# Kernel tuning notes

Hardware: AMD Instinct MI355X
Metric: run time of the kernel (lower is better)

The kernel has to match this reference:

```python
import jax, jax.numpy as jnp
import numpy as np

H = 12  # num_heads

def _alibi_bias(num_heads, n, dtype):
    # slopes: ratio**i for i in 1..H, ratio = 2**(-8/H)
    ratio = 2.0 ** (-8.0 / num_heads)
    slopes = ratio ** jnp.arange(1, num_heads + 1, dtype=jnp.float32)  # [H]
    pos = jnp.arange(n)
    rel = jnp.abs(pos[None, :] - pos[:, None]).astype(jnp.float32)  # [N,N]
    return (-slopes[:, None, None] * rel[None]).astype(dtype)  # [H,N,N]

def setup_inputs() -> dict:
    key = jax.random.key(0)
    ks = jax.random.split(key, 5)
    B, N, C = 16, 1024, 768
    s = 0.02
    return {
        "x": jax.random.normal(ks[0], (B, N, C), jnp.float32),
        "w_qkv": jax.random.normal(ks[1], (3 * C, C), jnp.float32) * s,
        "b_qkv": jax.random.normal(ks[2], (3 * C,), jnp.float32) * s,
        "w_proj": jax.random.normal(ks[3], (C, C), jnp.float32) * s,
        "b_proj": jax.random.normal(ks[4], (C,), jnp.float32) * s,
    }

def reference(x, w_qkv, b_qkv, w_proj, b_proj):
    B, N, C = x.shape
    D = C // H
    scale = D ** -0.5
    qkv = x @ w_qkv.T + b_qkv                       # [B,N,3C]
    qkv = qkv.reshape(B, N, 3, H, D)
    q = qkv[:, :, 0].transpose(0, 2, 1, 3)          # [B,H,N,D]
    k = qkv[:, :, 1].transpose(0, 2, 1, 3)
    v = qkv[:, :, 2].transpose(0, 2, 1, 3)
    bias = _alibi_bias(H, N, x.dtype)               # [H,N,N]
    scores = jnp.einsum('bhnd,bhmd->bhnm', q, k) * scale + bias[None]
    attn = jax.nn.softmax(scores, axis=-1)
    out = jnp.einsum('bhnm,bhmd->bhnd', attn, v)    # [B,H,N,D]
    out = out.transpose(0, 2, 1, 3).reshape(B, N, C)
    return out @ w_proj.T + b_proj
```

## Files before the change

### kernel.cpp

```cpp
#include <hip/hip_runtime.h>


typedef unsigned short u16;
typedef unsigned int u32;
typedef __attribute__((ext_vector_type(8))) short short8;
typedef __attribute__((ext_vector_type(4))) float f32x4;

__device__ __forceinline__ u16 f2bf(float f) {
    u32 u = __float_as_uint(f);
    u32 r = u + 0x7FFFu + ((u >> 16) & 1u);
    return (u16)(r >> 16);
}

__device__ __forceinline__ f32x4 mfma16(short8 a, short8 b, f32x4 c) {
    return __builtin_amdgcn_mfma_f32_16x16x32_bf16(a, b, c, 0, 0, 0);
}
__device__ __forceinline__ u32 cvtpk_bf16(float lo, float hi) {
    u32 r;
    asm("v_cvt_pk_bf16_f32 %0, %1, %2" : "=v"(r) : "v"(lo), "v"(hi));
    return r;
}

typedef __attribute__((address_space(1))) const unsigned int gu32_t;
typedef __attribute__((address_space(3))) unsigned int su32_t;
__device__ __forceinline__ void gl16(const u16* g, u16* s) {
    __builtin_amdgcn_global_load_lds((gu32_t*)g, (su32_t*)s, 16, 0, 0);
}

__global__ void cvt_all(const float* __restrict__ x, const float* __restrict__ wq,
                        const float* __restrict__ wp, u16* __restrict__ Xb,
                        u16* __restrict__ Wqkvb, u16* __restrict__ Wprojb) {
    int i = blockIdx.x * blockDim.x + threadIdx.x;
    int stride = gridDim.x * blockDim.x;
    for (int idx = i; idx < 3735552; idx += stride) {
        const float* src;
        u16* dst;
        int k;
        if (idx < 3145728) { src = x; dst = Xb; k = idx; }
        else if (idx < 3588096) { src = wq; dst = Wqkvb; k = idx - 3145728; }
        else { src = wp; dst = Wprojb; k = idx - 3588096; }
        float4 v = *(const float4*)(src + (size_t)k * 4);
        ushort4 o;
        o.x = f2bf(v.x); o.y = f2bf(v.y); o.z = f2bf(v.z); o.w = f2bf(v.w);
        *(ushort4*)(dst + (size_t)k * 4) = o;
    }
}

template <int EPI>
__global__ __launch_bounds__(512) void gemm_nt(
    const u16* __restrict__ A, const u16* __restrict__ Bw,
    const float* __restrict__ bias, u16* __restrict__ outb, float* __restrict__ outf,
    int nTilesN)
{
    constexpr int K = 768;
    constexpr int nkt = K / 32;
    __shared__ __align__(16) u16 lA[3][128 * 32];
    __shared__ __align__(16) u16 lB[3][128 * 32];

    int tid = threadIdx.x;
    int bid = blockIdx.x;
    int nwg = gridDim.x;
    int cpx = nwg >> 3;
    int swz = (bid & 7) * cpx + (bid >> 3);
    int bm = swz / nTilesN;
    int bn = swz - bm * nTilesN;
    int m0 = bm * 128, n0 = bn * 128;

    int sr = tid >> 2;
    int sc = (((tid & 3) ^ ((sr >> 1) & 3)) << 3);
    const u16* pA = A + (size_t)(m0 + sr) * K + sc;
    const u16* pB = Bw + (size_t)(n0 + sr) * K + sc;
    int lo = tid * 8;

    gl16(pA,      &lA[0][lo]);
    gl16(pB,      &lB[0][lo]);
    gl16(pA + 32, &lA[1][lo]);
    gl16(pB + 32, &lB[1][lo]);

    int w = tid >> 6, lane = tid & 63;
    int wm = w >> 2, wn = w & 3;
    int fq = lane >> 4, fr = lane & 15;
    int fsw = (fr >> 1) & 3;
    int colA = (fq ^ fsw) << 3;
    f32x4 acc[4][2] = {};

    for (int kt = 0; kt < nkt; ++kt) {
        int cur = kt % 3;
        if (kt < nkt - 1) { asm volatile("s_waitcnt vmcnt(2)" ::: "memory"); }
        else              { asm volatile("s_waitcnt vmcnt(0)" ::: "memory"); }
        __builtin_amdgcn_sched_barrier(0);
        __builtin_amdgcn_s_barrier();
        __builtin_amdgcn_sched_barrier(0);
        if (kt + 2 < nkt) {
            int nx = (kt + 2) % 3;
            gl16(pA + (kt + 2) * 32, &lA[nx][lo]);
            gl16(pB + (kt + 2) * 32, &lB[nx][lo]);
        }
        short8 af[4], bfr[2];
#pragma unroll
        for (int i = 0; i < 4; ++i)
            af[i] = *(const short8*)&lA[cur][(wm * 64 + i * 16 + fr) * 32 + colA];
#pragma unroll
        for (int j = 0; j < 2; ++j)
            bfr[j] = *(const short8*)&lB[cur][(wn * 32 + j * 16 + fr) * 32 + colA];
        __builtin_amdgcn_s_setprio(1);
#pragma unroll
        for (int i = 0; i < 4; ++i)
#pragma unroll
            for (int j = 0; j < 2; ++j)
                acc[i][j] = mfma16(af[i], bfr[j], acc[i][j]);
        __builtin_amdgcn_s_setprio(0);
    }

    if (EPI == 0) {
        int b = m0 >> 10;
        int i0 = (m0 & 1023) + wm * 64;
#pragma unroll
        for (int j = 0; j < 2; ++j) {
            int colb = n0 + wn * 32 + j * 16;
            int s = colb / 768;
            int rem = colb % 768;
            int hh = rem >> 6;
            int d0 = rem & 63;
            float bval = bias[colb + fr];
            u16* obase = outb + (((size_t)s * 16 + b) * 12 + hh) * 65536;
#pragma unroll
            for (int i = 0; i < 4; ++i) {
                int r0 = i0 + i * 16 + fq * 4;
#pragma unroll
                for (int r = 0; r < 4; ++r)
                    obase[(size_t)(r0 + r) * 64 + d0 + fr] = f2bf(acc[i][j][r] + bval);
            }
        }
    } else {
#pragma unroll
        for (int j = 0; j < 2; ++j) {
            int col = n0 + wn * 32 + j * 16 + fr;
            float bval = bias[col];
#pragma unroll
            for (int i = 0; i < 4; ++i) {
                int row0 = m0 + wm * 64 + i * 16 + fq * 4;
#pragma unroll
                for (int r = 0; r < 4; ++r)
                    outf[(size_t)(row0 + r) * 768 + col] = acc[i][j][r] + bval;
            }
        }
    }
}

__global__ __launch_bounds__(512) void attn_alibi(
    const u16* __restrict__ QKV, u16* __restrict__ att)
{
    int g = blockIdx.x;
    int xcd = g & 7;
    int idx = g >> 3;
    int qt = idx & 7;
    int bh = xcd * 24 + (idx >> 3);
    int h = bh % 12;
    int b = bh / 12;
    int q0 = qt * 128;
    const u16* Qg = QKV + (size_t)bh * 65536;
    const u16* Kg = QKV + (size_t)(192 + bh) * 65536;
    const u16* Vg = QKV + (size_t)(384 + bh) * 65536;

    __shared__ __align__(16) u16 Ks[64][72];
    __shared__ __align__(16) u16 Vt[64][72];
    __shared__ __align__(16) u16 Ps[128][72];

    int tid = threadIdx.x, w = tid >> 6, lane = tid & 63;
    int fq = lane >> 4, fr = lane & 15;

    short8 aq0 = *(const short8*)(Qg + (size_t)(q0 + w * 16 + fr) * 64 + fq * 8);
    short8 aq1 = *(const short8*)(Qg + (size_t)(q0 + w * 16 + fr) * 64 + 32 + fq * 8);

    const float C1 = 0.125f * 1.44269504f;
    float c2 = __builtin_amdgcn_exp2f(-(2.0f / 3.0f) * (float)(h + 1)) * 1.44269504f;
    int distThr = (int)(40.0f / c2);
    int lo_kv = q0 - 63 - distThr;
    int hi_kv = q0 + 127 + distThr;
    int t_lo = (lo_kv <= 0) ? 0 : (lo_kv >> 6);
    int t_hi = (hi_kv >= 1023) ? 15 : (hi_kv >> 6);

    bool isK = tid < 256;
    int t2 = tid & 255;
    int sr0 = t2 >> 3;
    int sc = (t2 & 7) * 8;
    int vswz = (t2 & 7) << 3;
    int vk0 = sr0 * 2;
    int vcol = vk0 ^ vswz;
    const u16* g0 = isK ? (Kg + (size_t)sr0 * 64 + sc)
                        : (Vg + (size_t)vk0 * 64 + sc);
    const u16* g1 = isK ? (Kg + (size_t)(sr0 + 32) * 64 + sc)
                        : (Vg + (size_t)(vk0 + 1) * 64 + sc);

    uint4 r0 = *(const uint4*)(g0 + (size_t)t_lo * 4096);
    uint4 r1 = *(const uint4*)(g1 + (size_t)t_lo * 4096);

    float di = (float)(q0 + w * 16 + fr - fq * 4);
    float lsum = 0.f;
    f32x4 acc[4] = {};

    for (int it = t_lo; it <= t_hi; ++it) {
        __syncthreads();
        if (isK) {
            *(uint4*)&Ks[sr0][sc] = r0;
            *(uint4*)&Ks[sr0 + 32][sc] = r1;
        } else {
            const u16* v0 = (const u16*)&r0;
            const u16* v1 = (const u16*)&r1;
#pragma unroll
            for (int jj = 0; jj < 8; ++jj)
                *(u32*)&Vt[sc + jj][vcol] = (u32)v0[jj] | ((u32)v1[jj] << 16);
        }
        __syncthreads();

        if (it < t_hi) {
            r0 = *(const uint4*)(g0 + (size_t)(it + 1) * 4096);
            r1 = *(const uint4*)(g1 + (size_t)(it + 1) * 4096);
        }

        f32x4 sfr[4];
        __builtin_amdgcn_s_setprio(1);
#pragma unroll
        for (int ct = 0; ct < 4; ++ct) {
            short8 bk0 = *(const short8*)&Ks[ct * 16 + fr][fq * 8];
            short8 bk1 = *(const short8*)&Ks[ct * 16 + fr][32 + fq * 8];
            f32x4 s0 = {0.f, 0.f, 0.f, 0.f};
            s0 = mfma16(bk0, aq0, s0);
            s0 = mfma16(bk1, aq1, s0);
            sfr[ct] = s0;
        }
        __builtin_amdgcn_s_setprio(0);

        float dkv = di - (float)(it * 64);
#pragma unroll
        for (int ct = 0; ct < 4; ++ct) {
            float t0 = dkv - (float)(ct * 16);
            float e0 = __builtin_amdgcn_exp2f(fmaf(sfr[ct][0], C1, -c2 * fabsf(t0)));
            float e1 = __builtin_amdgcn_exp2f(fmaf(sfr[ct][1], C1, -c2 * fabsf(t0 - 1.0f)));
            float e2 = __builtin_amdgcn_exp2f(fmaf(sfr[ct][2], C1, -c2 * fabsf(t0 - 2.0f)));
            float e3 = __builtin_amdgcn_exp2f(fmaf(sfr[ct][3], C1, -c2 * fabsf(t0 - 3.0f)));
            lsum += (e0 + e1) + (e2 + e3);
            uint2 pk;
            pk.x = cvtpk_bf16(e0, e1);
            pk.y = cvtpk_bf16(e2, e3);
            *(uint2*)&Ps[w * 16 + fr][ct * 16 + fq * 4] = pk;
        }

        short8 pa0 = *(const short8*)&Ps[w * 16 + fr][fq * 8];
        short8 pa1 = *(const short8*)&Ps[w * 16 + fr][32 + fq * 8];
        __builtin_amdgcn_s_setprio(1);
#pragma unroll
        for (int dt = 0; dt < 4; ++dt) {
            int row = dt * 16 + fr;
            int swzr = (row >> 3) << 3;
            short8 bv0 = *(const short8*)&Vt[row][(fq * 8) ^ swzr];
            short8 bv1 = *(const short8*)&Vt[row][(32 + fq * 8) ^ swzr];
            acc[dt] = mfma16(pa0, bv0, acc[dt]);
            acc[dt] = mfma16(pa1, bv1, acc[dt]);
        }
        __builtin_amdgcn_s_setprio(0);
    }

    float l = lsum;
    l += __shfl_xor(l, 16);
    l += __shfl_xor(l, 32);
    float rlo = 1.0f / l;
    float rl[4];
#pragma unroll
    for (int r = 0; r < 4; ++r)
        rl[r] = __shfl(rlo, fq * 4 + r);

#pragma unroll
    for (int dt = 0; dt < 4; ++dt)
#pragma unroll
        for (int r = 0; r < 4; ++r) {
            int ig = q0 + w * 16 + fq * 4 + r;
            att[((size_t)(b * 1024 + ig) * 12 + h) * 64 + dt * 16 + fr] =
                (u16)cvtpk_bf16(acc[dt][r] * rl[r], 0.f);
        }
}

extern "C" void kernel_launch(void* const* d_in, const int* in_sizes, int n_in,
                              void* d_out, int out_size, void* d_ws, size_t ws_size,
                              hipStream_t stream) {
    const float* x      = (const float*)d_in[0];
    const float* w_qkv  = (const float*)d_in[1];
    const float* b_qkv  = (const float*)d_in[2];
    const float* w_proj = (const float*)d_in[3];
    const float* b_proj = (const float*)d_in[4];
    float* out = (float*)d_out;

    char* ws = (char*)d_ws;
    u16* Xb     = (u16*)ws;
    u16* Wqkvb  = (u16*)(ws + 25165824);
    u16* Wprojb = (u16*)(ws + 28704768);
    u16* QKVb   = (u16*)(ws + 29884416);
    u16* Attb   = Xb;

    cvt_all<<<2048, 256, 0, stream>>>(x, w_qkv, w_proj, Xb, Wqkvb, Wprojb);

    gemm_nt<0><<<128 * 18, 512, 0, stream>>>(Xb, Wqkvb, b_qkv, QKVb, nullptr, 18);
    attn_alibi<<<1536, 512, 0, stream>>>(QKVb, Attb);
    gemm_nt<1><<<128 * 6, 512, 0, stream>>>(Attb, Wprojb, b_proj, nullptr, out, 6);
}
```

Measured before the change: 190.3 us.

## Fuse fp32-to-bf16 conversion of x and w_qkv into the QKV GEMM loads

Replaces the standalone conversion kernel for x and w_qkv with a QKV GEMM that loads fp32 tiles into registers, converts them to bf16, and stores them into double-buffered LDS. Only w_proj is still converted by a small separate kernel. This removes a full write and reread of the bf16 activation copy and one launch. In exchange the GEMM reads twice the bytes per tile from global memory and uses register-staged loads instead of direct global-to-LDS loads, which may hurt its pipelining.

Result: slower. 210.6 us (+10.7%).

```diff
diff --git a/kernel.cpp b/kernel.cpp
--- a/kernel.cpp
+++ b/kernel.cpp
@@ -27,22 +27,125 @@
     __builtin_amdgcn_global_load_lds((gu32_t*)g, (su32_t*)s, 16, 0, 0);
 }
 
-__global__ void cvt_all(const float* __restrict__ x, const float* __restrict__ wq,
-                        const float* __restrict__ wp, u16* __restrict__ Xb,
-                        u16* __restrict__ Wqkvb, u16* __restrict__ Wprojb) {
-    int i = blockIdx.x * blockDim.x + threadIdx.x;
-    int stride = gridDim.x * blockDim.x;
-    for (int idx = i; idx < 3735552; idx += stride) {
-        const float* src;
-        u16* dst;
-        int k;
-        if (idx < 3145728) { src = x; dst = Xb; k = idx; }
-        else if (idx < 3588096) { src = wq; dst = Wqkvb; k = idx - 3145728; }
-        else { src = wp; dst = Wprojb; k = idx - 3588096; }
-        float4 v = *(const float4*)(src + (size_t)k * 4);
-        ushort4 o;
-        o.x = f2bf(v.x); o.y = f2bf(v.y); o.z = f2bf(v.z); o.w = f2bf(v.w);
-        *(ushort4*)(dst + (size_t)k * 4) = o;
+__global__ void cvt_wp(const float* __restrict__ wp, u16* __restrict__ Wprojb) {
+    int idx = blockIdx.x * blockDim.x + threadIdx.x;
+    float4 v = *(const float4*)(wp + (size_t)idx * 4);
+    ushort4 o;
+    o.x = f2bf(v.x); o.y = f2bf(v.y); o.z = f2bf(v.z); o.w = f2bf(v.w);
+    *(ushort4*)(Wprojb + (size_t)idx * 4) = o;
+}
+
+__global__ __launch_bounds__(512) void gemm_qkv(
+    const float* __restrict__ A, const float* __restrict__ Bw,
+    const float* __restrict__ bias, u16* __restrict__ outb, int nTilesN)
+{
+    constexpr int K = 768;
+    constexpr int nkt = K / 32;
+    __shared__ __align__(16) u16 lA[2][128 * 32];
+    __shared__ __align__(16) u16 lB[2][128 * 32];
+
+    int tid = threadIdx.x;
+    int bid = blockIdx.x;
+    int nwg = gridDim.x;
+    int cpx = nwg >> 3;
+    int swz = (bid & 7) * cpx + (bid >> 3);
+    int bm = swz / nTilesN;
+    int bn = swz - bm * nTilesN;
+    int m0 = bm * 128, n0 = bn * 128;
+
+    int sr = tid >> 2;
+    int sc = (((tid & 3) ^ ((sr >> 1) & 3)) << 3);
+    const float* pA = A + (size_t)(m0 + sr) * K + sc;
+    const float* pB = Bw + (size_t)(n0 + sr) * K + sc;
+    int lo = tid * 8;
+
+    float4 a0 = *(const float4*)(pA);
+    float4 a1 = *(const float4*)(pA + 4);
+    float4 b0 = *(const float4*)(pB);
+    float4 b1 = *(const float4*)(pB + 4);
+    asm volatile("s_waitcnt vmcnt(0)" ::: "memory");
+    {
+        uint4 wa, wb;
+        wa.x = cvtpk_bf16(a0.x, a0.y); wa.y = cvtpk_bf16(a0.z, a0.w);
+        wa.z = cvtpk_bf16(a1.x, a1.y); wa.w = cvtpk_bf16(a1.z, a1.w);
+        wb.x = cvtpk_bf16(b0.x, b0.y); wb.y = cvtpk_bf16(b0.z, b0.w);
+        wb.z = cvtpk_bf16(b1.x, b1.y); wb.w = cvtpk_bf16(b1.z, b1.w);
+        *(uint4*)&lA[0][lo] = wa;
+        *(uint4*)&lB[0][lo] = wb;
+    }
+    a0 = *(const float4*)(pA + 32);
+    a1 = *(const float4*)(pA + 36);
+    b0 = *(const float4*)(pB + 32);
+    b1 = *(const float4*)(pB + 36);
+
+    int w = tid >> 6, lane = tid & 63;
+    int wm = w >> 2, wn = w & 3;
+    int fq = lane >> 4, fr = lane & 15;
+    int fsw = (fr >> 1) & 3;
+    int colA = (fq ^ fsw) << 3;
+    f32x4 acc[4][2] = {};
+
+    for (int kt = 0; kt < nkt; ++kt) {
+        int p = kt & 1;
+        asm volatile("s_waitcnt lgkmcnt(0)" ::: "memory");
+        __builtin_amdgcn_sched_barrier(0);
+        __builtin_amdgcn_s_barrier();
+        __builtin_amdgcn_sched_barrier(0);
+
+        short8 af[4], bfr[2];
+#pragma unroll
+        for (int i = 0; i < 4; ++i)
+            af[i] = *(const short8*)&lA[p][(wm * 64 + i * 16 + fr) * 32 + colA];
+#pragma unroll
+        for (int j = 0; j < 2; ++j)
+            bfr[j] = *(const short8*)&lB[p][(wn * 32 + j * 16 + fr) * 32 + colA];
+
+        if (kt + 1 < nkt) {
+            asm volatile("s_waitcnt vmcnt(0)" ::: "memory");
+            uint4 wa, wb;
+            wa.x = cvtpk_bf16(a0.x, a0.y); wa.y = cvtpk_bf16(a0.z, a0.w);
+            wa.z = cvtpk_bf16(a1.x, a1.y); wa.w = cvtpk_bf16(a1.z, a1.w);
+            wb.x = cvtpk_bf16(b0.x, b0.y); wb.y = cvtpk_bf16(b0.z, b0.w);
+            wb.z = cvtpk_bf16(b1.x, b1.y); wb.w = cvtpk_bf16(b1.z, b1.w);
+            *(uint4*)&lA[p ^ 1][lo] = wa;
+            *(uint4*)&lB[p ^ 1][lo] = wb;
+        }
+        if (kt + 2 < nkt) {
+            a0 = *(const float4*)(pA + (kt + 2) * 32);
+            a1 = *(const float4*)(pA + (kt + 2) * 32 + 4);
+            b0 = *(const float4*)(pB + (kt + 2) * 32);
+            b1 = *(const float4*)(pB + (kt + 2) * 32 + 4);
+        }
+
+        __builtin_amdgcn_s_setprio(1);
+#pragma unroll
+        for (int i = 0; i < 4; ++i)
+#pragma unroll
+            for (int j = 0; j < 2; ++j)
+                acc[i][j] = mfma16(af[i], bfr[j], acc[i][j]);
+        __builtin_amdgcn_s_setprio(0);
+    }
+
+    {
+        int b = m0 >> 10;
+        int i0 = (m0 & 1023) + wm * 64;
+#pragma unroll
+        for (int j = 0; j < 2; ++j) {
+            int colb = n0 + wn * 32 + j * 16;
+            int s = colb / 768;
+            int rem = colb % 768;
+            int hh = rem >> 6;
+            int d0 = rem & 63;
+            float bval = bias[colb + fr];
+            u16* obase = outb + (((size_t)s * 16 + b) * 12 + hh) * 65536;
+#pragma unroll
+            for (int i = 0; i < 4; ++i) {
+                int r0 = i0 + i * 16 + fq * 4;
+#pragma unroll
+                for (int r = 0; r < 4; ++r)
+                    obase[(size_t)(r0 + r) * 64 + d0 + fr] = f2bf(acc[i][j][r] + bval);
+            }
+        }
     }
 }
 
@@ -292,15 +395,13 @@
     float* out = (float*)d_out;
 
     char* ws = (char*)d_ws;
-    u16* Xb     = (u16*)ws;
-    u16* Wqkvb  = (u16*)(ws + 25165824);
+    u16* Attb   = (u16*)ws;
     u16* Wprojb = (u16*)(ws + 28704768);
     u16* QKVb   = (u16*)(ws + 29884416);
-    u16* Attb   = Xb;
-
-    cvt_all<<<2048, 256, 0, stream>>>(x, w_qkv, w_proj, Xb, Wqkvb, Wprojb);
-
-    gemm_nt<0><<<128 * 18, 512, 0, stream>>>(Xb, Wqkvb, b_qkv, QKVb, nullptr, 18);
+
+    cvt_wp<<<576, 256, 0, stream>>>(w_proj, Wprojb);
+
+    gemm_qkv<<<128 * 18, 512, 0, stream>>>(x, w_qkv, b_qkv, QKVb, 18);
     attn_alibi<<<1536, 512, 0, stream>>>(QKVb, Attb);
     gemm_nt<1><<<128 * 6, 512, 0, stream>>>(Attb, Wprojb, b_proj, nullptr, out, 6);
 }
```
